# Performance work log

Hardware: AMD Instinct MI355X
Metric: run time of the kernel (lower is better)

Reference implementation:

```python
import jax, jax.numpy as jnp
import numpy as np

HEADS = 8
NEG_SLOPE = 0.2  # PyG GATConv default LeakyReLU slope


def _gat_layer(x, src, dst, W, a_src, a_dst, bias, heads, out_ch):
    """PyG-style GATConv (concat heads, self-loops already appended, eval mode).
    x: [N, F_in]; src/dst: [E_tot] int; W: [F_in, heads*out_ch];
    a_src/a_dst: [heads, out_ch]; bias: [heads*out_ch].
    """
    N = x.shape[0]
    h = (x @ W).reshape(N, heads, out_ch)                      # [N, H, C]
    # per-node attention logits (gathered per edge as scalars, not features)
    al_s = jnp.einsum('nhc,hc->nh', h, a_src)                  # [N, H]
    al_d = jnp.einsum('nhc,hc->nh', h, a_dst)                  # [N, H]
    e = jax.nn.leaky_relu(al_s[src] + al_d[dst], negative_slope=NEG_SLOPE)  # [E, H]
    # segment softmax over incoming edges of each target node (stable)
    e_max = jax.ops.segment_max(e, dst, num_segments=N)        # self-loops => no empty segments
    ex = jnp.exp(e - e_max[dst])
    denom = jax.ops.segment_sum(ex, dst, num_segments=N)
    alpha = ex / (denom[dst] + 1e-16)                          # [E, H]
    # gather source features, weight, scatter-add to targets
    out = jax.ops.segment_sum(h[src] * alpha[:, :, None], dst, num_segments=N)  # [N, H, C]
    return out.reshape(N, heads * out_ch) + bias


def setup_inputs() -> dict:
    key = jax.random.key(0)
    ks = jax.random.split(key, 16)
    N, E, F_IN, NUM_CLASSES = 50000, 1600000, 128, 16
    s = 0.1
    return {
        'x': jax.random.normal(ks[0], (N, F_IN), dtype=jnp.float32),
        'edge_index': jax.random.randint(ks[1], (2, E), 0, N, dtype=jnp.int64),
        # GAT layer 1: 128 -> 8 heads x 8
        'W1': jax.random.normal(ks[2], (F_IN, 64), dtype=jnp.float32) * s,
        'a1_src': jax.random.normal(ks[3], (8, 8), dtype=jnp.float32) * s,
        'a1_dst': jax.random.normal(ks[4], (8, 8), dtype=jnp.float32) * s,
        'b1': jnp.zeros((64,), dtype=jnp.float32),
        # GAT layer 2: 64 -> 8 heads x 4
        'W2': jax.random.normal(ks[5], (64, 32), dtype=jnp.float32) * s,
        'a2_src': jax.random.normal(ks[6], (8, 4), dtype=jnp.float32) * s,
        'a2_dst': jax.random.normal(ks[7], (8, 4), dtype=jnp.float32) * s,
        'b2': jnp.zeros((32,), dtype=jnp.float32),
        # torch MultiheadAttention(32, 8): packed in_proj [96,32], out_proj [32,32]
        'in_proj_w': jax.random.normal(ks[8], (96, 32), dtype=jnp.float32) * s,
        'in_proj_b': jnp.zeros((96,), dtype=jnp.float32),
        'out_proj_w': jax.random.normal(ks[9], (32, 32), dtype=jnp.float32) * s,
        'out_proj_b': jnp.zeros((32,), dtype=jnp.float32),
        # fc: 32 -> num_classes
        'fc_w': jax.random.normal(ks[10], (NUM_CLASSES, 32), dtype=jnp.float32) * s,
        'fc_b': jnp.zeros((NUM_CLASSES,), dtype=jnp.float32),
    }


def reference(x, edge_index, W1, a1_src, a1_dst, b1, W2, a2_src, a2_dst, b2,
              in_proj_w, in_proj_b, out_proj_w, out_proj_b, fc_w, fc_b):
    N = x.shape[0]
    loops = jnp.arange(N, dtype=edge_index.dtype)
    src = jnp.concatenate([edge_index[0], loops])  # PyG add_self_loops=True
    dst = jnp.concatenate([edge_index[1], loops])

    h = jax.nn.elu(_gat_layer(x, src, dst, W1, a1_src, a1_dst, b1, HEADS, 8))   # [N, 64]
    h = jax.nn.elu(_gat_layer(h, src, dst, W2, a2_src, a2_dst, b2, HEADS, 4))   # [N, 32]

    # MultiheadAttention on h.unsqueeze(0): shape [1, N, 32] with torch's
    # seq-first layout => seq_len = 1, batch = N. Softmax over a single key
    # is identically 1 for every head, so out = out_proj(v_proj(h)).
    v = h @ in_proj_w[64:96].T + in_proj_b[64:96]   # v-projection slice of packed in_proj
    h = v @ out_proj_w.T + out_proj_b               # [N, 32]

    logits = h @ fc_w.T + fc_b                      # [N, num_classes]
    return jax.nn.log_softmax(logits, axis=1)
```

## Files before the change

### kernel.cpp

```cpp
#include <hip/hip_runtime.h>
#include <hip/hip_bf16.h>
#include <math.h>


#define BSHIFT 7
#define BMASK  ((1 << BSHIFT) - 1)
#define MAXNB  512
#define TILE   8192
#define XST    136
#define SMBYTES 36864

typedef __attribute__((ext_vector_type(8))) short short8;
typedef __attribute__((ext_vector_type(4))) float floatx4;
typedef __attribute__((ext_vector_type(2))) float floatx2;

__device__ __forceinline__ unsigned short f2bf(float f) {
    union { float f; unsigned int u; } v; v.f = f;
    unsigned int u = v.u;
    return (unsigned short)((u + 0x7FFFu + ((u >> 16) & 1u)) >> 16);
}
__device__ __forceinline__ float lrelu(float e) { return fmaxf(e, 0.2f * e); }
__device__ __forceinline__ float elu(float o) {
    return (o > 0.f) ? o : (__expf(o) - 1.f);
}

__global__ __launch_bounds__(256) void fused_pre_kernel(
    const float* __restrict__ x, const float* __restrict__ W,
    const float* __restrict__ a_src, const float* __restrict__ a_dst,
    char* __restrict__ rec1, float* __restrict__ ald, int N, int GB,
    const int* __restrict__ ei, int E, int Et, int NB, int CAP,
    int* __restrict__ gcount, unsigned int* __restrict__ rec, int NT,
    const float* __restrict__ in_proj_w, const float* __restrict__ in_proj_b,
    const float* __restrict__ out_proj_w, const float* __restrict__ out_proj_b,
    const float* __restrict__ fc_w, const float* __restrict__ fc_b,
    float* __restrict__ M, float* __restrict__ bf) {
    __shared__ __align__(16) char sm[SMBYTES];
    int t = threadIdx.x;
    int bid = blockIdx.x;
    if (bid < GB) {
        unsigned short* xs = (unsigned short*)sm;
        unsigned short* wt = xs + 64 * XST;
        int nb = bid * 64;
#pragma unroll
        for (int r = 0; r < 8; ++r) {
            int p = t + 256 * r;
            int row = p >> 5;
            int c4  = p & 31;
            int n = nb + row;
            float4 v = (n < N) ? ((const float4*)x)[(size_t)n * 32 + c4]
                               : make_float4(0.f, 0.f, 0.f, 0.f);
            unsigned short* dst = &xs[row * XST + c4 * 4];
            dst[0] = f2bf(v.x); dst[1] = f2bf(v.y);
            dst[2] = f2bf(v.z); dst[3] = f2bf(v.w);
        }
        {
            int n = t & 63, kg = t >> 6;
#pragma unroll
            for (int c = 0; c < 4; ++c) {
                int k0 = kg * 32 + c * 8;
                unsigned short* dst = &wt[n * XST + k0];
#pragma unroll
                for (int j = 0; j < 8; ++j)
                    dst[j] = f2bf(W[(k0 + j) * 64 + n]);
            }
        }
        __syncthreads();
        int wave = t >> 6, lane = t & 63;
        int m16 = lane & 15, quad = lane >> 4;
        floatx4 acc[4];
#pragma unroll
        for (int i = 0; i < 4; ++i) acc[i] = (floatx4){0.f, 0.f, 0.f, 0.f};
#pragma unroll
        for (int k = 0; k < 4; ++k) {
            int koff = k * 32 + quad * 8;
            short8 afrag = *(const short8*)&xs[(wave * 16 + m16) * XST + koff];
#pragma unroll
            for (int nt = 0; nt < 4; ++nt) {
                short8 bfrag = *(const short8*)&wt[(nt * 16 + m16) * XST + koff];
                acc[nt] = __builtin_amdgcn_mfma_f32_16x16x32_bf16(afrag, bfrag, acc[nt], 0, 0, 0);
            }
        }
        __syncthreads();
        float* hs = (float*)sm;
#pragma unroll
        for (int nt = 0; nt < 4; ++nt)
#pragma unroll
            for (int r = 0; r < 4; ++r)
                hs[(wave * 16 + quad * 4 + r) * 65 + nt * 16 + m16] = acc[nt][r];
        __syncthreads();
        float asv = a_src[lane], adv = a_dst[lane];
        for (int itn = 0; itn < 16; ++itn) {
            int nl = wave * 16 + itn;
            int n = nb + nl;
            if (n >= N) break;
            float v = hs[nl * 65 + lane];
            float ps = v * asv, pd = v * adv;
            ps += __shfl_xor(ps, 1); ps += __shfl_xor(ps, 2); ps += __shfl_xor(ps, 4);
            pd += __shfl_xor(pd, 1); pd += __shfl_xor(pd, 2); pd += __shfl_xor(pd, 4);
            if ((lane & 7) == 0) {
                *(float*)(rec1 + (size_t)n * 128 + 4 * (lane >> 3)) = ps;
                ald[n * 8 + (lane >> 3)] = pd;
            }
            if (lane < 16) {
                const float* hr = &hs[nl * 65 + lane * 4];
                int pk = __builtin_amdgcn_cvt_pk_fp8_f32(hr[0], hr[1], 0, false);
                pk = __builtin_amdgcn_cvt_pk_fp8_f32(hr[2], hr[3], pk, true);
                *(unsigned*)(rec1 + (size_t)n * 128 + 64 + 4 * lane) = (unsigned)pk;
            }
        }
    } else if (bid < GB + NT) {
        unsigned int* lrec = (unsigned int*)sm;
        int* h   = (int*)(sm + TILE * 4);
        int* cur = (int*)(sm + TILE * 4 + MAXNB * 4);
        for (int i = t; i < NB; i += 256) h[i] = 0;
        int tile0 = (bid - GB) * TILE;
        int cnt = Et - tile0; if (cnt > TILE) cnt = TILE;
        __syncthreads();
        for (int j = t; j < cnt; j += 256) {
            int jj = tile0 + j;
            int srcv, d;
            if (jj < E) { srcv = ei[jj]; d = ei[E + jj]; } else { srcv = jj - E; d = jj - E; }
            lrec[j] = (unsigned)srcv | ((unsigned)d << 16);
            atomicAdd(&h[d >> BSHIFT], 1);
        }
        __syncthreads();
        for (int i = t; i < NB; i += 256)
            cur[i] = h[i] ? atomicAdd(&gcount[i], h[i]) : 0;
        __syncthreads();
        for (int j = t; j < cnt; j += 256) {
            unsigned v = lrec[j];
            int b = v >> (16 + BSHIFT);
            int pos = atomicAdd(&cur[b], 1);
            if (pos < CAP)
                rec[(size_t)b * CAP + pos] =
                    (v & 0xFFFFu) | ((((v >> 16) & BMASK)) << 16);
        }
    } else {
        float* Wvo = (float*)sm;
        float* bvo = (float*)(sm + 4096);
        const float* Wv = in_proj_w + 64 * 32;
        const float* bv = in_proj_b + 64;
        for (int idx = t; idx < 1024; idx += 256) {
            int i = idx >> 5, j = idx & 31;
            float acc = 0.f;
            for (int k = 0; k < 32; ++k) acc += out_proj_w[i * 32 + k] * Wv[k * 32 + j];
            Wvo[idx] = acc;
        }
        if (t < 32) {
            float acc = 0.f;
            for (int k = 0; k < 32; ++k) acc += out_proj_w[t * 32 + k] * bv[k];
            bvo[t] = acc + out_proj_b[t];
        }
        __syncthreads();
        for (int idx = t; idx < 16 * 32; idx += 256) {
            int cc = idx >> 5, j = idx & 31;
            float acc = 0.f;
            for (int i = 0; i < 32; ++i) acc += fc_w[cc * 32 + i] * Wvo[i * 32 + j];
            M[idx] = acc;
        }
        if (t < 16) {
            float acc = 0.f;
            for (int i = 0; i < 32; ++i) acc += fc_w[t * 32 + i] * bvo[i];
            bf[t] = acc + fc_b[t];
        }
    }
}

__global__ __launch_bounds__(256) void csr_finalize_kernel(
    const unsigned int* __restrict__ rec, const int* __restrict__ gcount,
    int* __restrict__ rowp, unsigned short* __restrict__ esrc,
    int N, int Et, int CAP) {
    __shared__ int h[128];
    __shared__ int nb[128];
    __shared__ int cur[128];
    __shared__ int ssum[256];
    int b = blockIdx.x, t = threadIdx.x;
    size_t rbase = (size_t)b * CAP;
    int cnt = gcount[b]; if (cnt > CAP) cnt = CAP;
    if (t < 128) h[t] = 0;
    int acc = 0;
    for (int i = t; i < b; i += 256) {
        int v = gcount[i];
        acc += (v < CAP) ? v : CAP;
    }
    ssum[t] = acc;
    __syncthreads();
    for (int off = 128; off >= 1; off >>= 1) {
        if (t < off) ssum[t] += ssum[t + off];
        __syncthreads();
    }
    int obase = ssum[0];
    for (int i = t; i < cnt; i += 256)
        atomicAdd(&h[(rec[rbase + i] >> 16) & 127], 1);
    __syncthreads();
    if (t == 0) {
        int run = obase;
        for (int i = 0; i < 128; ++i) { nb[i] = run; run += h[i]; }
    }
    __syncthreads();
    if (t < 128) cur[t] = nb[t];
    int n0 = b << BSHIFT;
    if (t < 128 && n0 + t < N) rowp[n0 + t] = nb[t];
    if (b == 0 && t == 0) rowp[N] = Et;
    __syncthreads();
    for (int i = t; i < cnt; i += 256) {
        unsigned r = rec[rbase + i];
        int pos = atomicAdd(&cur[(r >> 16) & 127], 1);
        esrc[pos] = (unsigned short)(r & 0xFFFFu);
    }
}

__global__ __launch_bounds__(256) void gat_agg64_g2_kernel(
    const int* __restrict__ rowp, const unsigned short* __restrict__ esrc,
    const char* __restrict__ rec1, const float* __restrict__ ald_arr,
    const float* __restrict__ bias,
    const float* __restrict__ W2, const float* __restrict__ a2s,
    const float* __restrict__ a2d,
    char* __restrict__ rec2, float* __restrict__ ald2, int N) {
    __shared__ __align__(16) float W2p[2][8][32][4];
    __shared__ __align__(16) float oL[4][64];
    __shared__ __align__(16) float h2L[4][32];
    int t = threadIdx.x;
    for (int idx = t; idx < 2048; idx += 256) {
        int k = idx >> 5, l = idx & 31;
        W2p[k >> 5][(k & 31) >> 2][l][k & 3] = W2[idx];
    }
    __syncthreads();
    const int lane = t & 63;
    const int wv = t >> 6;
    const int e = lane >> 4;
    const int c = lane & 15;
    const int hd = c >> 1;
    const int aoff = 4 * hd;
    const int foff = 64 + 4 * c;
    int n = blockIdx.x * 4 + wv;
    if (n >= N) return;
    float aldv = ald_arr[n * 8 + hd];
    int beg = rowp[n], end = rowp[n + 1];
    float dA = 0.f, dB = 0.f;
    floatx2 p0a = {0.f, 0.f}, p0b = {0.f, 0.f};
    floatx2 p1a = {0.f, 0.f}, p1b = {0.f, 0.f};
    floatx2 p2a = {0.f, 0.f}, p2b = {0.f, 0.f};
    floatx2 p3a = {0.f, 0.f}, p3b = {0.f, 0.f};
    int i = beg;
    for (; i + 32 <= end; i += 32) {
        int s0 = esrc[i + e],      s1 = esrc[i + 4 + e];
        int s2 = esrc[i + 8 + e],  s3 = esrc[i + 12 + e];
        int s4 = esrc[i + 16 + e], s5 = esrc[i + 20 + e];
        int s6 = esrc[i + 24 + e], s7 = esrc[i + 28 + e];
        const char* r0 = rec1 + (size_t)s0 * 128;
        const char* r1 = rec1 + (size_t)s1 * 128;
        const char* r2 = rec1 + (size_t)s2 * 128;
        const char* r3 = rec1 + (size_t)s3 * 128;
        const char* r4 = rec1 + (size_t)s4 * 128;
        const char* r5 = rec1 + (size_t)s5 * 128;
        const char* r6 = rec1 + (size_t)s6 * 128;
        const char* r7 = rec1 + (size_t)s7 * 128;
        float e0 = *(const float*)(r0 + aoff), e1 = *(const float*)(r1 + aoff);
        float e2 = *(const float*)(r2 + aoff), e3 = *(const float*)(r3 + aoff);
        float e4 = *(const float*)(r4 + aoff), e5 = *(const float*)(r5 + aoff);
        float e6 = *(const float*)(r6 + aoff), e7 = *(const float*)(r7 + aoff);
        unsigned g0 = *(const unsigned*)(r0 + foff), g1 = *(const unsigned*)(r1 + foff);
        unsigned g2 = *(const unsigned*)(r2 + foff), g3 = *(const unsigned*)(r3 + foff);
        unsigned g4 = *(const unsigned*)(r4 + foff), g5 = *(const unsigned*)(r5 + foff);
        unsigned g6 = *(const unsigned*)(r6 + foff), g7 = *(const unsigned*)(r7 + foff);
        float w0 = __expf(lrelu(e0 + aldv));
        float w1 = __expf(lrelu(e1 + aldv));
        float w2 = __expf(lrelu(e2 + aldv));
        float w3 = __expf(lrelu(e3 + aldv));
        float w4 = __expf(lrelu(e4 + aldv));
        float w5 = __expf(lrelu(e5 + aldv));
        float w6 = __expf(lrelu(e6 + aldv));
        float w7 = __expf(lrelu(e7 + aldv));
        dA += w0 + w2; dB += w1 + w3;
        dA += w4 + w6; dB += w5 + w7;
        p0a += w0 * __builtin_amdgcn_cvt_pk_f32_fp8(g0, false);
        p0b += w0 * __builtin_amdgcn_cvt_pk_f32_fp8(g0, true);
        p1a += w1 * __builtin_amdgcn_cvt_pk_f32_fp8(g1, false);
        p1b += w1 * __builtin_amdgcn_cvt_pk_f32_fp8(g1, true);
        p2a += w2 * __builtin_amdgcn_cvt_pk_f32_fp8(g2, false);
        p2b += w2 * __builtin_amdgcn_cvt_pk_f32_fp8(g2, true);
        p3a += w3 * __builtin_amdgcn_cvt_pk_f32_fp8(g3, false);
        p3b += w3 * __builtin_amdgcn_cvt_pk_f32_fp8(g3, true);
        p0a += w4 * __builtin_amdgcn_cvt_pk_f32_fp8(g4, false);
        p0b += w4 * __builtin_amdgcn_cvt_pk_f32_fp8(g4, true);
        p1a += w5 * __builtin_amdgcn_cvt_pk_f32_fp8(g5, false);
        p1b += w5 * __builtin_amdgcn_cvt_pk_f32_fp8(g5, true);
        p2a += w6 * __builtin_amdgcn_cvt_pk_f32_fp8(g6, false);
        p2b += w6 * __builtin_amdgcn_cvt_pk_f32_fp8(g6, true);
        p3a += w7 * __builtin_amdgcn_cvt_pk_f32_fp8(g7, false);
        p3b += w7 * __builtin_amdgcn_cvt_pk_f32_fp8(g7, true);
    }
    for (; i < end; i += 16) {
        int i0 = i + e, i1 = i + 4 + e, i2 = i + 8 + e, i3 = i + 12 + e;
        bool v0 = i0 < end, v1 = i1 < end, v2 = i2 < end, v3 = i3 < end;
        int c0 = v0 ? i0 : beg;
        int c1 = v1 ? i1 : beg;
        int c2 = v2 ? i2 : beg;
        int c3 = v3 ? i3 : beg;
        int s0 = esrc[c0], s1 = esrc[c1], s2 = esrc[c2], s3 = esrc[c3];
        const char* r0 = rec1 + (size_t)s0 * 128;
        const char* r1 = rec1 + (size_t)s1 * 128;
        const char* r2 = rec1 + (size_t)s2 * 128;
        const char* r3 = rec1 + (size_t)s3 * 128;
        float e0 = *(const float*)(r0 + aoff), e1 = *(const float*)(r1 + aoff);
        float e2 = *(const float*)(r2 + aoff), e3 = *(const float*)(r3 + aoff);
        unsigned g0 = *(const unsigned*)(r0 + foff), g1 = *(const unsigned*)(r1 + foff);
        unsigned g2 = *(const unsigned*)(r2 + foff), g3 = *(const unsigned*)(r3 + foff);
        float w0 = v0 ? __expf(lrelu(e0 + aldv)) : 0.f;
        float w1 = v1 ? __expf(lrelu(e1 + aldv)) : 0.f;
        float w2 = v2 ? __expf(lrelu(e2 + aldv)) : 0.f;
        float w3 = v3 ? __expf(lrelu(e3 + aldv)) : 0.f;
        dA += w0 + w2; dB += w1 + w3;
        p0a += w0 * __builtin_amdgcn_cvt_pk_f32_fp8(g0, false);
        p0b += w0 * __builtin_amdgcn_cvt_pk_f32_fp8(g0, true);
        p1a += w1 * __builtin_amdgcn_cvt_pk_f32_fp8(g1, false);
        p1b += w1 * __builtin_amdgcn_cvt_pk_f32_fp8(g1, true);
        p2a += w2 * __builtin_amdgcn_cvt_pk_f32_fp8(g2, false);
        p2b += w2 * __builtin_amdgcn_cvt_pk_f32_fp8(g2, true);
        p3a += w3 * __builtin_amdgcn_cvt_pk_f32_fp8(g3, false);
        p3b += w3 * __builtin_amdgcn_cvt_pk_f32_fp8(g3, true);
    }
    float d = dA + dB;
    floatx2 Pa = (p0a + p1a) + (p2a + p3a);
    floatx2 Pb = (p0b + p1b) + (p2b + p3b);
    float P0 = Pa.x, P1 = Pa.y, P2 = Pb.x, P3 = Pb.y;
    d  += __shfl_xor(d, 16);  d  += __shfl_xor(d, 32);
    P0 += __shfl_xor(P0, 16); P0 += __shfl_xor(P0, 32);
    P1 += __shfl_xor(P1, 16); P1 += __shfl_xor(P1, 32);
    P2 += __shfl_xor(P2, 16); P2 += __shfl_xor(P2, 32);
    P3 += __shfl_xor(P3, 16); P3 += __shfl_xor(P3, 32);
    float inv = 1.f / (d + 1e-16f);
    float4 bv = ((const float4*)bias)[c];
    float o0 = elu(P0 * inv + bv.x);
    float o1 = elu(P1 * inv + bv.y);
    float o2 = elu(P2 * inv + bv.z);
    float o3 = elu(P3 * inv + bv.w);
    if (lane < 16) *(float4*)&oL[wv][c * 4] = make_float4(o0, o1, o2, o3);
    const int l = lane & 31, kh = lane >> 5;
    const float* orow = &oL[wv][kh * 32];
    float a0 = 0.f, a1 = 0.f, a2 = 0.f, a3 = 0.f;
#pragma unroll
    for (int g = 0; g < 8; ++g) {
        float4 ov = *(const float4*)&orow[g * 4];
        float4 wv4 = *(const float4*)&W2p[kh][g][l][0];
        a0 += ov.x * wv4.x; a1 += ov.y * wv4.y;
        a2 += ov.z * wv4.z; a3 += ov.w * wv4.w;
    }
    float acc = (a0 + a1) + (a2 + a3);
    acc += __shfl_xor(acc, 32);
    float ps = acc * a2s[l], pd = acc * a2d[l];
    ps += __shfl_xor(ps, 1); ps += __shfl_xor(ps, 2);
    pd += __shfl_xor(pd, 1); pd += __shfl_xor(pd, 2);
    if (lane < 32) {
        h2L[wv][l] = acc;
        if ((l & 3) == 0) {
            *(float*)(rec2 + (size_t)n * 64 + 4 * (l >> 2)) = ps;
            ald2[n * 8 + (l >> 2)] = pd;
        }
    }
    if (lane < 8) {
        const float* hr = &h2L[wv][lane * 4];
        int pk = __builtin_amdgcn_cvt_pk_fp8_f32(hr[0], hr[1], 0, false);
        pk = __builtin_amdgcn_cvt_pk_fp8_f32(hr[2], hr[3], pk, true);
        *(unsigned*)(rec2 + (size_t)n * 64 + 32 + 4 * lane) = (unsigned)pk;
    }
}

__global__ __launch_bounds__(256) void gat_agg32_fin_kernel(
    const int* __restrict__ rowp, const unsigned short* __restrict__ esrc,
    const char* __restrict__ rec2, const float* __restrict__ ald_arr,
    const float* __restrict__ bias,
    const float* __restrict__ M, const float* __restrict__ bf,
    float* __restrict__ out, int N) {
    __shared__ __align__(16) float Mp[8][16][4];
    __shared__ float bfs[16];
    __shared__ __align__(16) float oL[4][32];
    int t = threadIdx.x;
    for (int i = t; i < 512; i += 256) {
        int j = i >> 5, k = i & 31;
        Mp[k >> 2][j][k & 3] = M[i];
    }
    if (t < 16) bfs[t] = bf[t];
    __syncthreads();
    const int lane = t & 63;
    const int wv = t >> 6;
    const int e = lane >> 3;
    const int c = lane & 7;
    const int aoff = 4 * c;
    const int foff = 32 + 4 * c;
    int n = blockIdx.x * 4 + wv;
    if (n >= N) return;
    float aldv = ald_arr[n * 8 + c];
    int beg = rowp[n], end = rowp[n + 1];
    float d0 = 0.f, d1 = 0.f, d2 = 0.f, d3 = 0.f;
    floatx2 p0a = {0.f, 0.f}, p0b = {0.f, 0.f};
    floatx2 p1a = {0.f, 0.f}, p1b = {0.f, 0.f};
    floatx2 p2a = {0.f, 0.f}, p2b = {0.f, 0.f};
    floatx2 p3a = {0.f, 0.f}, p3b = {0.f, 0.f};
    int base = beg;
    for (; base + 32 <= end; base += 32) {
        int s0 = esrc[base + e],      s1 = esrc[base + 8 + e];
        int s2 = esrc[base + 16 + e], s3 = esrc[base + 24 + e];
        const char* r0 = rec2 + (size_t)s0 * 64;
        const char* r1 = rec2 + (size_t)s1 * 64;
        const char* r2 = rec2 + (size_t)s2 * 64;
        const char* r3 = rec2 + (size_t)s3 * 64;
        float e0 = *(const float*)(r0 + aoff) + aldv;
        float e1 = *(const float*)(r1 + aoff) + aldv;
        float e2 = *(const float*)(r2 + aoff) + aldv;
        float e3 = *(const float*)(r3 + aoff) + aldv;
        unsigned g0 = *(const unsigned*)(r0 + foff);
        unsigned g1 = *(const unsigned*)(r1 + foff);
        unsigned g2 = *(const unsigned*)(r2 + foff);
        unsigned g3 = *(const unsigned*)(r3 + foff);
        float w0 = __expf(lrelu(e0));
        float w1 = __expf(lrelu(e1));
        float w2 = __expf(lrelu(e2));
        float w3 = __expf(lrelu(e3));
        d0 += w0; d1 += w1; d2 += w2; d3 += w3;
        p0a += w0 * __builtin_amdgcn_cvt_pk_f32_fp8(g0, false);
        p0b += w0 * __builtin_amdgcn_cvt_pk_f32_fp8(g0, true);
        p1a += w1 * __builtin_amdgcn_cvt_pk_f32_fp8(g1, false);
        p1b += w1 * __builtin_amdgcn_cvt_pk_f32_fp8(g1, true);
        p2a += w2 * __builtin_amdgcn_cvt_pk_f32_fp8(g2, false);
        p2b += w2 * __builtin_amdgcn_cvt_pk_f32_fp8(g2, true);
        p3a += w3 * __builtin_amdgcn_cvt_pk_f32_fp8(g3, false);
        p3b += w3 * __builtin_amdgcn_cvt_pk_f32_fp8(g3, true);
    }
    for (; base < end; base += 32) {
        int i0 = base + e;
        int i1 = base + 8 + e;
        int i2 = base + 16 + e;
        int i3 = base + 24 + e;
        bool v0 = i0 < end, v1 = i1 < end, v2 = i2 < end, v3 = i3 < end;
        int c0 = v0 ? i0 : beg;
        int c1 = v1 ? i1 : beg;
        int c2 = v2 ? i2 : beg;
        int c3 = v3 ? i3 : beg;
        int s0 = esrc[c0], s1 = esrc[c1], s2 = esrc[c2], s3 = esrc[c3];
        const char* r0 = rec2 + (size_t)s0 * 64;
        const char* r1 = rec2 + (size_t)s1 * 64;
        const char* r2 = rec2 + (size_t)s2 * 64;
        const char* r3 = rec2 + (size_t)s3 * 64;
        float e0 = *(const float*)(r0 + aoff) + aldv;
        float e1 = *(const float*)(r1 + aoff) + aldv;
        float e2 = *(const float*)(r2 + aoff) + aldv;
        float e3 = *(const float*)(r3 + aoff) + aldv;
        unsigned g0 = *(const unsigned*)(r0 + foff);
        unsigned g1 = *(const unsigned*)(r1 + foff);
        unsigned g2 = *(const unsigned*)(r2 + foff);
        unsigned g3 = *(const unsigned*)(r3 + foff);
        float w0 = v0 ? __expf(lrelu(e0)) : 0.f;
        float w1 = v1 ? __expf(lrelu(e1)) : 0.f;
        float w2 = v2 ? __expf(lrelu(e2)) : 0.f;
        float w3 = v3 ? __expf(lrelu(e3)) : 0.f;
        d0 += w0; d1 += w1; d2 += w2; d3 += w3;
        p0a += w0 * __builtin_amdgcn_cvt_pk_f32_fp8(g0, false);
        p0b += w0 * __builtin_amdgcn_cvt_pk_f32_fp8(g0, true);
        p1a += w1 * __builtin_amdgcn_cvt_pk_f32_fp8(g1, false);
        p1b += w1 * __builtin_amdgcn_cvt_pk_f32_fp8(g1, true);
        p2a += w2 * __builtin_amdgcn_cvt_pk_f32_fp8(g2, false);
        p2b += w2 * __builtin_amdgcn_cvt_pk_f32_fp8(g2, true);
        p3a += w3 * __builtin_amdgcn_cvt_pk_f32_fp8(g3, false);
        p3b += w3 * __builtin_amdgcn_cvt_pk_f32_fp8(g3, true);
    }
    float d = (d0 + d1) + (d2 + d3);
    floatx2 Pa = (p0a + p1a) + (p2a + p3a);
    floatx2 Pb = (p0b + p1b) + (p2b + p3b);
    float P0 = Pa.x, P1 = Pa.y, P2 = Pb.x, P3 = Pb.y;
    d  += __shfl_xor(d, 8);  d  += __shfl_xor(d, 16);  d  += __shfl_xor(d, 32);
    P0 += __shfl_xor(P0, 8); P0 += __shfl_xor(P0, 16); P0 += __shfl_xor(P0, 32);
    P1 += __shfl_xor(P1, 8); P1 += __shfl_xor(P1, 16); P1 += __shfl_xor(P1, 32);
    P2 += __shfl_xor(P2, 8); P2 += __shfl_xor(P2, 16); P2 += __shfl_xor(P2, 32);
    P3 += __shfl_xor(P3, 8); P3 += __shfl_xor(P3, 16); P3 += __shfl_xor(P3, 32);
    float inv = 1.f / (d + 1e-16f);
    float4 bv = ((const float4*)bias)[c];
    float o0 = elu(P0 * inv + bv.x);
    float o1 = elu(P1 * inv + bv.y);
    float o2 = elu(P2 * inv + bv.z);
    float o3 = elu(P3 * inv + bv.w);
    if (lane < 8) *(float4*)&oL[wv][c * 4] = make_float4(o0, o1, o2, o3);
    const int j = lane & 15;
    const float* orow = oL[wv];
    float a0 = 0.f, a1 = 0.f, a2 = 0.f, a3 = 0.f;
#pragma unroll
    for (int g = 0; g < 8; ++g) {
        float4 ov = *(const float4*)&orow[g * 4];
        float4 mv = *(const float4*)&Mp[g][j][0];
        a0 += ov.x * mv.x; a1 += ov.y * mv.y;
        a2 += ov.z * mv.z; a3 += ov.w * mv.w;
    }
    float logit = (a0 + a1) + (a2 + a3) + bfs[j];
    float mx = logit;
    mx = fmaxf(mx, __shfl_xor(mx, 1));
    mx = fmaxf(mx, __shfl_xor(mx, 2));
    mx = fmaxf(mx, __shfl_xor(mx, 4));
    mx = fmaxf(mx, __shfl_xor(mx, 8));
    float ex = __expf(logit - mx);
    float se = ex;
    se += __shfl_xor(se, 1);
    se += __shfl_xor(se, 2);
    se += __shfl_xor(se, 4);
    se += __shfl_xor(se, 8);
    float res = logit - (mx + __logf(se));
    if (lane < 16) out[(size_t)n * 16 + j] = res;
}

extern "C" void kernel_launch(void* const* d_in, const int* in_sizes, int n_in,
                              void* d_out, int out_size, void* d_ws, size_t ws_size,
                              hipStream_t stream) {
    const float* x   = (const float*)d_in[0];
    const int*   ei  = (const int*)d_in[1];
    const float* W1  = (const float*)d_in[2];
    const float* a1s = (const float*)d_in[3];
    const float* a1d = (const float*)d_in[4];
    const float* b1  = (const float*)d_in[5];
    const float* W2  = (const float*)d_in[6];
    const float* a2s = (const float*)d_in[7];
    const float* a2d = (const float*)d_in[8];
    const float* b2  = (const float*)d_in[9];
    const float* ipw = (const float*)d_in[10];
    const float* ipb = (const float*)d_in[11];
    const float* opw = (const float*)d_in[12];
    const float* opb = (const float*)d_in[13];
    const float* fcw = (const float*)d_in[14];
    const float* fcb = (const float*)d_in[15];
    float* out = (float*)d_out;

    int N = in_sizes[0] / 128;
    int E = in_sizes[1] / 2;
    int Et = E + N;
    int NB = (N + BMASK) >> BSHIFT;
    int NTILES = (Et + TILE - 1) / TILE;
    int GB = (N + 63) / 64;
    int CAP = Et / NB;
    CAP = CAP + CAP / 8 + 256;
    CAP = (CAP + 255) & ~255;

    char* ws = (char*)d_ws;
    size_t off = 0;
    auto alloc = [&](size_t bytes) -> void* {
        void* p = ws + off;
        off += bytes;
        off = (off + 255) & ~(size_t)255;
        return p;
    };
    int*   bcount = (int*)alloc(MAXNB * 4);
    unsigned int*   rec  = (unsigned int*)alloc((size_t)NB * CAP * 4);
    int*   rowp   = (int*)alloc((size_t)(N + 1) * 4);
    unsigned short* esrc = (unsigned short*)alloc((size_t)Et * 2);
    char* rec1   = (char*)alloc((size_t)N * 128);
    float* al1d  = (float*)alloc((size_t)N * 8 * 4);
    char* rec2   = (char*)alloc((size_t)N * 64);
    float* al2d  = (float*)alloc((size_t)N * 8 * 4);
    float* Mf    = (float*)alloc(512 * 4);
    float* bff   = (float*)alloc(16 * 4);
    (void)ws_size; (void)n_in; (void)out_size;

    hipMemsetAsync(bcount, 0, MAXNB * 4, stream);
    fused_pre_kernel<<<GB + NTILES + 1, 256, 0, stream>>>(
        x, W1, a1s, a1d, rec1, al1d, N, GB,
        ei, E, Et, NB, CAP, bcount, rec, NTILES,
        ipw, ipb, opw, opb, fcw, fcb, Mf, bff);
    csr_finalize_kernel<<<NB, 256, 0, stream>>>(rec, bcount, rowp, esrc, N, Et, CAP);

    gat_agg64_g2_kernel<<<(N + 3) / 4, 256, 0, stream>>>(
        rowp, esrc, rec1, al1d, b1, W2, a2s, a2d, rec2, al2d, N);
    gat_agg32_fin_kernel<<<(N + 3) / 4, 256, 0, stream>>>(
        rowp, esrc, rec2, al2d, b2, Mf, bff, out, N);
}
```

Before: 211.9 us.

## Split layer-1 node records, stage CSR scatter in LDS, add low-degree fast paths

Layer-1 per-node data moves from one interleaved 128-byte record into separate arrays for the source logits and the packed fp8 features. The CSR finalize step now sorts edge sources into a shared-memory buffer and writes them out contiguously instead of scattering straight to global memory. Both aggregation kernels gain a fully unrolled path for nodes of degree up to 48 or 64 that issues all gathers at once for more memory-level parallelism. The LDS buffer caps the per-bucket CAP, so an overfull bucket could lose edges, and the unrolled paths raise register use.

```diff
diff --git a/kernel.cpp b/kernel.cpp
--- a/kernel.cpp
+++ b/kernel.cpp
@@ -9,6 +9,7 @@
 #define TILE   8192
 #define XST    136
 #define SMBYTES 36864
+#define LESRC_MAX 6144
 
 typedef __attribute__((ext_vector_type(8))) short short8;
 typedef __attribute__((ext_vector_type(4))) float floatx4;
@@ -27,7 +28,8 @@
 __global__ __launch_bounds__(256) void fused_pre_kernel(
     const float* __restrict__ x, const float* __restrict__ W,
     const float* __restrict__ a_src, const float* __restrict__ a_dst,
-    char* __restrict__ rec1, float* __restrict__ ald, int N, int GB,
+    unsigned int* __restrict__ h1p, float* __restrict__ als,
+    float* __restrict__ ald, int N, int GB,
     const int* __restrict__ ei, int E, int Et, int NB, int CAP,
     int* __restrict__ gcount, unsigned int* __restrict__ rec, int NT,
     const float* __restrict__ in_proj_w, const float* __restrict__ in_proj_b,
@@ -98,14 +100,14 @@
             ps += __shfl_xor(ps, 1); ps += __shfl_xor(ps, 2); ps += __shfl_xor(ps, 4);
             pd += __shfl_xor(pd, 1); pd += __shfl_xor(pd, 2); pd += __shfl_xor(pd, 4);
             if ((lane & 7) == 0) {
-                *(float*)(rec1 + (size_t)n * 128 + 4 * (lane >> 3)) = ps;
+                als[n * 8 + (lane >> 3)] = ps;
                 ald[n * 8 + (lane >> 3)] = pd;
             }
             if (lane < 16) {
                 const float* hr = &hs[nl * 65 + lane * 4];
                 int pk = __builtin_amdgcn_cvt_pk_fp8_f32(hr[0], hr[1], 0, false);
                 pk = __builtin_amdgcn_cvt_pk_fp8_f32(hr[2], hr[3], pk, true);
-                *(unsigned*)(rec1 + (size_t)n * 128 + 64 + 4 * lane) = (unsigned)pk;
+                h1p[(size_t)n * 16 + lane] = (unsigned)pk;
             }
         }
     } else if (bid < GB + NT) {
@@ -174,6 +176,7 @@
     __shared__ int nb[128];
     __shared__ int cur[128];
     __shared__ int ssum[256];
+    __shared__ unsigned short lesrc[LESRC_MAX];
     int b = blockIdx.x, t = threadIdx.x;
     size_t rbase = (size_t)b * CAP;
     int cnt = gcount[b]; if (cnt > CAP) cnt = CAP;
@@ -194,26 +197,29 @@
         atomicAdd(&h[(rec[rbase + i] >> 16) & 127], 1);
     __syncthreads();
     if (t == 0) {
-        int run = obase;
+        int run = 0;
         for (int i = 0; i < 128; ++i) { nb[i] = run; run += h[i]; }
     }
     __syncthreads();
     if (t < 128) cur[t] = nb[t];
     int n0 = b << BSHIFT;
-    if (t < 128 && n0 + t < N) rowp[n0 + t] = nb[t];
+    if (t < 128 && n0 + t < N) rowp[n0 + t] = obase + nb[t];
     if (b == 0 && t == 0) rowp[N] = Et;
     __syncthreads();
     for (int i = t; i < cnt; i += 256) {
         unsigned r = rec[rbase + i];
         int pos = atomicAdd(&cur[(r >> 16) & 127], 1);
-        esrc[pos] = (unsigned short)(r & 0xFFFFu);
-    }
+        lesrc[pos] = (unsigned short)(r & 0xFFFFu);
+    }
+    __syncthreads();
+    for (int i = t; i < cnt; i += 256)
+        esrc[obase + i] = lesrc[i];
 }
 
 __global__ __launch_bounds__(256) void gat_agg64_g2_kernel(
     const int* __restrict__ rowp, const unsigned short* __restrict__ esrc,
-    const char* __restrict__ rec1, const float* __restrict__ ald_arr,
-    const float* __restrict__ bias,
+    const unsigned int* __restrict__ feat, const float* __restrict__ als,
+    const float* __restrict__ ald_arr, const float* __restrict__ bias,
     const float* __restrict__ W2, const float* __restrict__ a2s,
     const float* __restrict__ a2d,
     char* __restrict__ rec2, float* __restrict__ ald2, int N) {
@@ -231,95 +237,120 @@
     const int e = lane >> 4;
     const int c = lane & 15;
     const int hd = c >> 1;
-    const int aoff = 4 * hd;
-    const int foff = 64 + 4 * c;
     int n = blockIdx.x * 4 + wv;
     if (n >= N) return;
     float aldv = ald_arr[n * 8 + hd];
     int beg = rowp[n], end = rowp[n + 1];
+    int deg = end - beg;
     float dA = 0.f, dB = 0.f;
     floatx2 p0a = {0.f, 0.f}, p0b = {0.f, 0.f};
     floatx2 p1a = {0.f, 0.f}, p1b = {0.f, 0.f};
     floatx2 p2a = {0.f, 0.f}, p2b = {0.f, 0.f};
     floatx2 p3a = {0.f, 0.f}, p3b = {0.f, 0.f};
-    int i = beg;
-    for (; i + 32 <= end; i += 32) {
-        int s0 = esrc[i + e],      s1 = esrc[i + 4 + e];
-        int s2 = esrc[i + 8 + e],  s3 = esrc[i + 12 + e];
-        int s4 = esrc[i + 16 + e], s5 = esrc[i + 20 + e];
-        int s6 = esrc[i + 24 + e], s7 = esrc[i + 28 + e];
-        const char* r0 = rec1 + (size_t)s0 * 128;
-        const char* r1 = rec1 + (size_t)s1 * 128;
-        const char* r2 = rec1 + (size_t)s2 * 128;
-        const char* r3 = rec1 + (size_t)s3 * 128;
-        const char* r4 = rec1 + (size_t)s4 * 128;
-        const char* r5 = rec1 + (size_t)s5 * 128;
-        const char* r6 = rec1 + (size_t)s6 * 128;
-        const char* r7 = rec1 + (size_t)s7 * 128;
-        float e0 = *(const float*)(r0 + aoff), e1 = *(const float*)(r1 + aoff);
-        float e2 = *(const float*)(r2 + aoff), e3 = *(const float*)(r3 + aoff);
-        float e4 = *(const float*)(r4 + aoff), e5 = *(const float*)(r5 + aoff);
-        float e6 = *(const float*)(r6 + aoff), e7 = *(const float*)(r7 + aoff);
-        unsigned g0 = *(const unsigned*)(r0 + foff), g1 = *(const unsigned*)(r1 + foff);
-        unsigned g2 = *(const unsigned*)(r2 + foff), g3 = *(const unsigned*)(r3 + foff);
-        unsigned g4 = *(const unsigned*)(r4 + foff), g5 = *(const unsigned*)(r5 + foff);
-        unsigned g6 = *(const unsigned*)(r6 + foff), g7 = *(const unsigned*)(r7 + foff);
-        float w0 = __expf(lrelu(e0 + aldv));
-        float w1 = __expf(lrelu(e1 + aldv));
-        float w2 = __expf(lrelu(e2 + aldv));
-        float w3 = __expf(lrelu(e3 + aldv));
-        float w4 = __expf(lrelu(e4 + aldv));
-        float w5 = __expf(lrelu(e5 + aldv));
-        float w6 = __expf(lrelu(e6 + aldv));
-        float w7 = __expf(lrelu(e7 + aldv));
-        dA += w0 + w2; dB += w1 + w3;
-        dA += w4 + w6; dB += w5 + w7;
-        p0a += w0 * __builtin_amdgcn_cvt_pk_f32_fp8(g0, false);
-        p0b += w0 * __builtin_amdgcn_cvt_pk_f32_fp8(g0, true);
-        p1a += w1 * __builtin_amdgcn_cvt_pk_f32_fp8(g1, false);
-        p1b += w1 * __builtin_amdgcn_cvt_pk_f32_fp8(g1, true);
-        p2a += w2 * __builtin_amdgcn_cvt_pk_f32_fp8(g2, false);
-        p2b += w2 * __builtin_amdgcn_cvt_pk_f32_fp8(g2, true);
-        p3a += w3 * __builtin_amdgcn_cvt_pk_f32_fp8(g3, false);
-        p3b += w3 * __builtin_amdgcn_cvt_pk_f32_fp8(g3, true);
-        p0a += w4 * __builtin_amdgcn_cvt_pk_f32_fp8(g4, false);
-        p0b += w4 * __builtin_amdgcn_cvt_pk_f32_fp8(g4, true);
-        p1a += w5 * __builtin_amdgcn_cvt_pk_f32_fp8(g5, false);
-        p1b += w5 * __builtin_amdgcn_cvt_pk_f32_fp8(g5, true);
-        p2a += w6 * __builtin_amdgcn_cvt_pk_f32_fp8(g6, false);
-        p2b += w6 * __builtin_amdgcn_cvt_pk_f32_fp8(g6, true);
-        p3a += w7 * __builtin_amdgcn_cvt_pk_f32_fp8(g7, false);
-        p3b += w7 * __builtin_amdgcn_cvt_pk_f32_fp8(g7, true);
-    }
-    for (; i < end; i += 16) {
-        int i0 = i + e, i1 = i + 4 + e, i2 = i + 8 + e, i3 = i + 12 + e;
-        bool v0 = i0 < end, v1 = i1 < end, v2 = i2 < end, v3 = i3 < end;
-        int c0 = v0 ? i0 : beg;
-        int c1 = v1 ? i1 : beg;
-        int c2 = v2 ? i2 : beg;
-        int c3 = v3 ? i3 : beg;
-        int s0 = esrc[c0], s1 = esrc[c1], s2 = esrc[c2], s3 = esrc[c3];
-        const char* r0 = rec1 + (size_t)s0 * 128;
-        const char* r1 = rec1 + (size_t)s1 * 128;
-        const char* r2 = rec1 + (size_t)s2 * 128;
-        const char* r3 = rec1 + (size_t)s3 * 128;
-        float e0 = *(const float*)(r0 + aoff), e1 = *(const float*)(r1 + aoff);
-        float e2 = *(const float*)(r2 + aoff), e3 = *(const float*)(r3 + aoff);
-        unsigned g0 = *(const unsigned*)(r0 + foff), g1 = *(const unsigned*)(r1 + foff);
-        unsigned g2 = *(const unsigned*)(r2 + foff), g3 = *(const unsigned*)(r3 + foff);
-        float w0 = v0 ? __expf(lrelu(e0 + aldv)) : 0.f;
-        float w1 = v1 ? __expf(lrelu(e1 + aldv)) : 0.f;
-        float w2 = v2 ? __expf(lrelu(e2 + aldv)) : 0.f;
-        float w3 = v3 ? __expf(lrelu(e3 + aldv)) : 0.f;
-        dA += w0 + w2; dB += w1 + w3;
-        p0a += w0 * __builtin_amdgcn_cvt_pk_f32_fp8(g0, false);
-        p0b += w0 * __builtin_amdgcn_cvt_pk_f32_fp8(g0, true);
-        p1a += w1 * __builtin_amdgcn_cvt_pk_f32_fp8(g1, false);
-        p1b += w1 * __builtin_amdgcn_cvt_pk_f32_fp8(g1, true);
-        p2a += w2 * __builtin_amdgcn_cvt_pk_f32_fp8(g2, false);
-        p2b += w2 * __builtin_amdgcn_cvt_pk_f32_fp8(g2, true);
-        p3a += w3 * __builtin_amdgcn_cvt_pk_f32_fp8(g3, false);
-        p3b += w3 * __builtin_amdgcn_cvt_pk_f32_fp8(g3, true);
+    if (deg <= 48) {
+        int s[12];
+#pragma unroll
+        for (int g = 0; g < 12; ++g) {
+            int p = beg + g * 4 + e;
+            s[g] = esrc[(p < end) ? p : beg];
+        }
+        float ev[12];
+        unsigned gg[12];
+#pragma unroll
+        for (int g = 0; g < 12; ++g) {
+            ev[g] = als[s[g] * 8 + hd];
+            gg[g] = feat[s[g] * 16 + c];
+        }
+#pragma unroll
+        for (int g = 0; g < 12; ++g) {
+            bool vv = (beg + g * 4 + e) < end;
+            float w = vv ? __expf(lrelu(ev[g] + aldv)) : 0.f;
+            if ((g & 3) == 0) {
+                dA += w;
+                p0a += w * __builtin_amdgcn_cvt_pk_f32_fp8(gg[g], false);
+                p0b += w * __builtin_amdgcn_cvt_pk_f32_fp8(gg[g], true);
+            } else if ((g & 3) == 1) {
+                dB += w;
+                p1a += w * __builtin_amdgcn_cvt_pk_f32_fp8(gg[g], false);
+                p1b += w * __builtin_amdgcn_cvt_pk_f32_fp8(gg[g], true);
+            } else if ((g & 3) == 2) {
+                dA += w;
+                p2a += w * __builtin_amdgcn_cvt_pk_f32_fp8(gg[g], false);
+                p2b += w * __builtin_amdgcn_cvt_pk_f32_fp8(gg[g], true);
+            } else {
+                dB += w;
+                p3a += w * __builtin_amdgcn_cvt_pk_f32_fp8(gg[g], false);
+                p3b += w * __builtin_amdgcn_cvt_pk_f32_fp8(gg[g], true);
+            }
+        }
+    } else {
+        int i = beg;
+        for (; i + 32 <= end; i += 32) {
+            int s0 = esrc[i + e],      s1 = esrc[i + 4 + e];
+            int s2 = esrc[i + 8 + e],  s3 = esrc[i + 12 + e];
+            int s4 = esrc[i + 16 + e], s5 = esrc[i + 20 + e];
+            int s6 = esrc[i + 24 + e], s7 = esrc[i + 28 + e];
+            float e0 = als[s0 * 8 + hd], e1 = als[s1 * 8 + hd];
+            float e2 = als[s2 * 8 + hd], e3 = als[s3 * 8 + hd];
+            float e4 = als[s4 * 8 + hd], e5 = als[s5 * 8 + hd];
+            float e6 = als[s6 * 8 + hd], e7 = als[s7 * 8 + hd];
+            unsigned g0 = feat[s0 * 16 + c], g1 = feat[s1 * 16 + c];
+            unsigned g2 = feat[s2 * 16 + c], g3 = feat[s3 * 16 + c];
+            unsigned g4 = feat[s4 * 16 + c], g5 = feat[s5 * 16 + c];
+            unsigned g6 = feat[s6 * 16 + c], g7 = feat[s7 * 16 + c];
+            float w0 = __expf(lrelu(e0 + aldv));
+            float w1 = __expf(lrelu(e1 + aldv));
+            float w2 = __expf(lrelu(e2 + aldv));
+            float w3 = __expf(lrelu(e3 + aldv));
+            float w4 = __expf(lrelu(e4 + aldv));
+            float w5 = __expf(lrelu(e5 + aldv));
+            float w6 = __expf(lrelu(e6 + aldv));
+            float w7 = __expf(lrelu(e7 + aldv));
+            dA += w0 + w2; dB += w1 + w3;
+            dA += w4 + w6; dB += w5 + w7;
+            p0a += w0 * __builtin_amdgcn_cvt_pk_f32_fp8(g0, false);
+            p0b += w0 * __builtin_amdgcn_cvt_pk_f32_fp8(g0, true);
+            p1a += w1 * __builtin_amdgcn_cvt_pk_f32_fp8(g1, false);
+            p1b += w1 * __builtin_amdgcn_cvt_pk_f32_fp8(g1, true);
+            p2a += w2 * __builtin_amdgcn_cvt_pk_f32_fp8(g2, false);
+            p2b += w2 * __builtin_amdgcn_cvt_pk_f32_fp8(g2, true);
+            p3a += w3 * __builtin_amdgcn_cvt_pk_f32_fp8(g3, false);
+            p3b += w3 * __builtin_amdgcn_cvt_pk_f32_fp8(g3, true);
+            p0a += w4 * __builtin_amdgcn_cvt_pk_f32_fp8(g4, false);
+            p0b += w4 * __builtin_amdgcn_cvt_pk_f32_fp8(g4, true);
+            p1a += w5 * __builtin_amdgcn_cvt_pk_f32_fp8(g5, false);
+            p1b += w5 * __builtin_amdgcn_cvt_pk_f32_fp8(g5, true);
+            p2a += w6 * __builtin_amdgcn_cvt_pk_f32_fp8(g6, false);
+            p2b += w6 * __builtin_amdgcn_cvt_pk_f32_fp8(g6, true);
+            p3a += w7 * __builtin_amdgcn_cvt_pk_f32_fp8(g7, false);
+            p3b += w7 * __builtin_amdgcn_cvt_pk_f32_fp8(g7, true);
+        }
+        for (; i < end; i += 16) {
+            int i0 = i + e, i1 = i + 4 + e, i2 = i + 8 + e, i3 = i + 12 + e;
+            bool v0 = i0 < end, v1 = i1 < end, v2 = i2 < end, v3 = i3 < end;
+            int c0 = v0 ? i0 : beg;
+            int c1 = v1 ? i1 : beg;
+            int c2 = v2 ? i2 : beg;
+            int c3 = v3 ? i3 : beg;
+            int s0 = esrc[c0], s1 = esrc[c1], s2 = esrc[c2], s3 = esrc[c3];
+            float e0 = als[s0 * 8 + hd], e1 = als[s1 * 8 + hd];
+            float e2 = als[s2 * 8 + hd], e3 = als[s3 * 8 + hd];
+            unsigned g0 = feat[s0 * 16 + c], g1 = feat[s1 * 16 + c];
+            unsigned g2 = feat[s2 * 16 + c], g3 = feat[s3 * 16 + c];
+            float w0 = v0 ? __expf(lrelu(e0 + aldv)) : 0.f;
+            float w1 = v1 ? __expf(lrelu(e1 + aldv)) : 0.f;
+            float w2 = v2 ? __expf(lrelu(e2 + aldv)) : 0.f;
+            float w3 = v3 ? __expf(lrelu(e3 + aldv)) : 0.f;
+            dA += w0 + w2; dB += w1 + w3;
+            p0a += w0 * __builtin_amdgcn_cvt_pk_f32_fp8(g0, false);
+            p0b += w0 * __builtin_amdgcn_cvt_pk_f32_fp8(g0, true);
+            p1a += w1 * __builtin_amdgcn_cvt_pk_f32_fp8(g1, false);
+            p1b += w1 * __builtin_amdgcn_cvt_pk_f32_fp8(g1, true);
+            p2a += w2 * __builtin_amdgcn_cvt_pk_f32_fp8(g2, false);
+            p2b += w2 * __builtin_amdgcn_cvt_pk_f32_fp8(g2, true);
+            p3a += w3 * __builtin_amdgcn_cvt_pk_f32_fp8(g3, false);
+            p3b += w3 * __builtin_amdgcn_cvt_pk_f32_fp8(g3, true);
+        }
     }
     float d = dA + dB;
     floatx2 Pa = (p0a + p1a) + (p2a + p3a);
@@ -393,77 +424,117 @@
     if (n >= N) return;
     float aldv = ald_arr[n * 8 + c];
     int beg = rowp[n], end = rowp[n + 1];
+    int deg = end - beg;
     float d0 = 0.f, d1 = 0.f, d2 = 0.f, d3 = 0.f;
     floatx2 p0a = {0.f, 0.f}, p0b = {0.f, 0.f};
     floatx2 p1a = {0.f, 0.f}, p1b = {0.f, 0.f};
     floatx2 p2a = {0.f, 0.f}, p2b = {0.f, 0.f};
     floatx2 p3a = {0.f, 0.f}, p3b = {0.f, 0.f};
-    int base = beg;
-    for (; base + 32 <= end; base += 32) {
-        int s0 = esrc[base + e],      s1 = esrc[base + 8 + e];
-        int s2 = esrc[base + 16 + e], s3 = esrc[base + 24 + e];
-        const char* r0 = rec2 + (size_t)s0 * 64;
-        const char* r1 = rec2 + (size_t)s1 * 64;
-        const char* r2 = rec2 + (size_t)s2 * 64;
-        const char* r3 = rec2 + (size_t)s3 * 64;
-        float e0 = *(const float*)(r0 + aoff) + aldv;
-        float e1 = *(const float*)(r1 + aoff) + aldv;
-        float e2 = *(const float*)(r2 + aoff) + aldv;
-        float e3 = *(const float*)(r3 + aoff) + aldv;
-        unsigned g0 = *(const unsigned*)(r0 + foff);
-        unsigned g1 = *(const unsigned*)(r1 + foff);
-        unsigned g2 = *(const unsigned*)(r2 + foff);
-        unsigned g3 = *(const unsigned*)(r3 + foff);
-        float w0 = __expf(lrelu(e0));
-        float w1 = __expf(lrelu(e1));
-        float w2 = __expf(lrelu(e2));
-        float w3 = __expf(lrelu(e3));
-        d0 += w0; d1 += w1; d2 += w2; d3 += w3;
-        p0a += w0 * __builtin_amdgcn_cvt_pk_f32_fp8(g0, false);
-        p0b += w0 * __builtin_amdgcn_cvt_pk_f32_fp8(g0, true);
-        p1a += w1 * __builtin_amdgcn_cvt_pk_f32_fp8(g1, false);
-        p1b += w1 * __builtin_amdgcn_cvt_pk_f32_fp8(g1, true);
-        p2a += w2 * __builtin_amdgcn_cvt_pk_f32_fp8(g2, false);
-        p2b += w2 * __builtin_amdgcn_cvt_pk_f32_fp8(g2, true);
-        p3a += w3 * __builtin_amdgcn_cvt_pk_f32_fp8(g3, false);
-        p3b += w3 * __builtin_amdgcn_cvt_pk_f32_fp8(g3, true);
-    }
-    for (; base < end; base += 32) {
-        int i0 = base + e;
-        int i1 = base + 8 + e;
-        int i2 = base + 16 + e;
-        int i3 = base + 24 + e;
-        bool v0 = i0 < end, v1 = i1 < end, v2 = i2 < end, v3 = i3 < end;
-        int c0 = v0 ? i0 : beg;
-        int c1 = v1 ? i1 : beg;
-        int c2 = v2 ? i2 : beg;
-        int c3 = v3 ? i3 : beg;
-        int s0 = esrc[c0], s1 = esrc[c1], s2 = esrc[c2], s3 = esrc[c3];
-        const char* r0 = rec2 + (size_t)s0 * 64;
-        const char* r1 = rec2 + (size_t)s1 * 64;
-        const char* r2 = rec2 + (size_t)s2 * 64;
-        const char* r3 = rec2 + (size_t)s3 * 64;
-        float e0 = *(const float*)(r0 + aoff) + aldv;
-        float e1 = *(const float*)(r1 + aoff) + aldv;
-        float e2 = *(const float*)(r2 + aoff) + aldv;
-        float e3 = *(const float*)(r3 + aoff) + aldv;
-        unsigned g0 = *(const unsigned*)(r0 + foff);
-        unsigned g1 = *(const unsigned*)(r1 + foff);
-        unsigned g2 = *(const unsigned*)(r2 + foff);
-        unsigned g3 = *(const unsigned*)(r3 + foff);
-        float w0 = v0 ? __expf(lrelu(e0)) : 0.f;
-        float w1 = v1 ? __expf(lrelu(e1)) : 0.f;
-        float w2 = v2 ? __expf(lrelu(e2)) : 0.f;
-        float w3 = v3 ? __expf(lrelu(e3)) : 0.f;
-        d0 += w0; d1 += w1; d2 += w2; d3 += w3;
-        p0a += w0 * __builtin_amdgcn_cvt_pk_f32_fp8(g0, false);
-        p0b += w0 * __builtin_amdgcn_cvt_pk_f32_fp8(g0, true);
-        p1a += w1 * __builtin_amdgcn_cvt_pk_f32_fp8(g1, false);
-        p1b += w1 * __builtin_amdgcn_cvt_pk_f32_fp8(g1, true);
-        p2a += w2 * __builtin_amdgcn_cvt_pk_f32_fp8(g2, false);
-        p2b += w2 * __builtin_amdgcn_cvt_pk_f32_fp8(g2, true);
-        p3a += w3 * __builtin_amdgcn_cvt_pk_f32_fp8(g3, false);
-        p3b += w3 * __builtin_amdgcn_cvt_pk_f32_fp8(g3, true);
+    if (deg <= 64) {
+        int s[8];
+#pragma unroll
+        for (int g = 0; g < 8; ++g) {
+            int p = beg + g * 8 + e;
+            s[g] = esrc[(p < end) ? p : beg];
+        }
+        float ev[8];
+        unsigned gg[8];
+#pragma unroll
+        for (int g = 0; g < 8; ++g) {
+            const char* r = rec2 + (size_t)s[g] * 64;
+            ev[g] = *(const float*)(r + aoff);
+            gg[g] = *(const unsigned*)(r + foff);
+        }
+#pragma unroll
+        for (int g = 0; g < 8; ++g) {
+            bool vv = (beg + g * 8 + e) < end;
+            float w = vv ? __expf(lrelu(ev[g] + aldv)) : 0.f;
+            if ((g & 3) == 0) {
+                d0 += w;
+                p0a += w * __builtin_amdgcn_cvt_pk_f32_fp8(gg[g], false);
+                p0b += w * __builtin_amdgcn_cvt_pk_f32_fp8(gg[g], true);
+            } else if ((g & 3) == 1) {
+                d1 += w;
+                p1a += w * __builtin_amdgcn_cvt_pk_f32_fp8(gg[g], false);
+                p1b += w * __builtin_amdgcn_cvt_pk_f32_fp8(gg[g], true);
+            } else if ((g & 3) == 2) {
+                d2 += w;
+                p2a += w * __builtin_amdgcn_cvt_pk_f32_fp8(gg[g], false);
+                p2b += w * __builtin_amdgcn_cvt_pk_f32_fp8(gg[g], true);
+            } else {
+                d3 += w;
+                p3a += w * __builtin_amdgcn_cvt_pk_f32_fp8(gg[g], false);
+                p3b += w * __builtin_amdgcn_cvt_pk_f32_fp8(gg[g], true);
+            }
+        }
+    } else {
+        int base = beg;
+        for (; base + 32 <= end; base += 32) {
+            int s0 = esrc[base + e],      s1 = esrc[base + 8 + e];
+            int s2 = esrc[base + 16 + e], s3 = esrc[base + 24 + e];
+            const char* r0 = rec2 + (size_t)s0 * 64;
+            const char* r1 = rec2 + (size_t)s1 * 64;
+            const char* r2 = rec2 + (size_t)s2 * 64;
+            const char* r3 = rec2 + (size_t)s3 * 64;
+            float e0 = *(const float*)(r0 + aoff) + aldv;
+            float e1 = *(const float*)(r1 + aoff) + aldv;
+            float e2 = *(const float*)(r2 + aoff) + aldv;
+            float e3 = *(const float*)(r3 + aoff) + aldv;
+            unsigned g0 = *(const unsigned*)(r0 + foff);
+            unsigned g1 = *(const unsigned*)(r1 + foff);
+            unsigned g2 = *(const unsigned*)(r2 + foff);
+            unsigned g3 = *(const unsigned*)(r3 + foff);
+            float w0 = __expf(lrelu(e0));
+            float w1 = __expf(lrelu(e1));
+            float w2 = __expf(lrelu(e2));
+            float w3 = __expf(lrelu(e3));
+            d0 += w0; d1 += w1; d2 += w2; d3 += w3;
+            p0a += w0 * __builtin_amdgcn_cvt_pk_f32_fp8(g0, false);
+            p0b += w0 * __builtin_amdgcn_cvt_pk_f32_fp8(g0, true);
+            p1a += w1 * __builtin_amdgcn_cvt_pk_f32_fp8(g1, false);
+            p1b += w1 * __builtin_amdgcn_cvt_pk_f32_fp8(g1, true);
+            p2a += w2 * __builtin_amdgcn_cvt_pk_f32_fp8(g2, false);
+            p2b += w2 * __builtin_amdgcn_cvt_pk_f32_fp8(g2, true);
+            p3a += w3 * __builtin_amdgcn_cvt_pk_f32_fp8(g3, false);
+            p3b += w3 * __builtin_amdgcn_cvt_pk_f32_fp8(g3, true);
+        }
+        for (; base < end; base += 32) {
+            int i0 = base + e;
+            int i1 = base + 8 + e;
+            int i2 = base + 16 + e;
+            int i3 = base + 24 + e;
+            bool v0 = i0 < end, v1 = i1 < end, v2 = i2 < end, v3 = i3 < end;
+            int c0 = v0 ? i0 : beg;
+            int c1 = v1 ? i1 : beg;
+            int c2 = v2 ? i2 : beg;
+            int c3 = v3 ? i3 : beg;
+            int s0 = esrc[c0], s1 = esrc[c1], s2 = esrc[c2], s3 = esrc[c3];
+            const char* r0 = rec2 + (size_t)s0 * 64;
+            const char* r1 = rec2 + (size_t)s1 * 64;
+            const char* r2 = rec2 + (size_t)s2 * 64;
+            const char* r3 = rec2 + (size_t)s3 * 64;
+            float e0 = *(const float*)(r0 + aoff) + aldv;
+            float e1 = *(const float*)(r1 + aoff) + aldv;
+            float e2 = *(const float*)(r2 + aoff) + aldv;
+            float e3 = *(const float*)(r3 + aoff) + aldv;
+            unsigned g0 = *(const unsigned*)(r0 + foff);
+            unsigned g1 = *(const unsigned*)(r1 + foff);
+            unsigned g2 = *(const unsigned*)(r2 + foff);
+            unsigned g3 = *(const unsigned*)(r3 + foff);
+            float w0 = v0 ? __expf(lrelu(e0)) : 0.f;
+            float w1 = v1 ? __expf(lrelu(e1)) : 0.f;
+            float w2 = v2 ? __expf(lrelu(e2)) : 0.f;
+            float w3 = v3 ? __expf(lrelu(e3)) : 0.f;
+            d0 += w0; d1 += w1; d2 += w2; d3 += w3;
+            p0a += w0 * __builtin_amdgcn_cvt_pk_f32_fp8(g0, false);
+            p0b += w0 * __builtin_amdgcn_cvt_pk_f32_fp8(g0, true);
+            p1a += w1 * __builtin_amdgcn_cvt_pk_f32_fp8(g1, false);
+            p1b += w1 * __builtin_amdgcn_cvt_pk_f32_fp8(g1, true);
+            p2a += w2 * __builtin_amdgcn_cvt_pk_f32_fp8(g2, false);
+            p2b += w2 * __builtin_amdgcn_cvt_pk_f32_fp8(g2, true);
+            p3a += w3 * __builtin_amdgcn_cvt_pk_f32_fp8(g3, false);
+            p3b += w3 * __builtin_amdgcn_cvt_pk_f32_fp8(g3, true);
+        }
     }
     float d = (d0 + d1) + (d2 + d3);
     floatx2 Pa = (p0a + p1a) + (p2a + p3a);
@@ -537,6 +608,7 @@
     int CAP = Et / NB;
     CAP = CAP + CAP / 8 + 256;
     CAP = (CAP + 255) & ~255;
+    if (CAP > LESRC_MAX) CAP = LESRC_MAX;
 
     char* ws = (char*)d_ws;
     size_t off = 0;
@@ -550,7 +622,8 @@
     unsigned int*   rec  = (unsigned int*)alloc((size_t)NB * CAP * 4);
     int*   rowp   = (int*)alloc((size_t)(N + 1) * 4);
     unsigned short* esrc = (unsigned short*)alloc((size_t)Et * 2);
-    char* rec1   = (char*)alloc((size_t)N * 128);
+    unsigned int* h1p = (unsigned int*)alloc((size_t)N * 16 * 4);
+    float* al1s  = (float*)alloc((size_t)N * 8 * 4);
     float* al1d  = (float*)alloc((size_t)N * 8 * 4);
     char* rec2   = (char*)alloc((size_t)N * 64);
     float* al2d  = (float*)alloc((size_t)N * 8 * 4);
@@ -560,13 +633,13 @@
 
     hipMemsetAsync(bcount, 0, MAXNB * 4, stream);
     fused_pre_kernel<<<GB + NTILES + 1, 256, 0, stream>>>(
-        x, W1, a1s, a1d, rec1, al1d, N, GB,
+        x, W1, a1s, a1d, h1p, al1s, al1d, N, GB,
         ei, E, Et, NB, CAP, bcount, rec, NTILES,
         ipw, ipb, opw, opb, fcw, fcb, Mf, bff);
     csr_finalize_kernel<<<NB, 256, 0, stream>>>(rec, bcount, rowp, esrc, N, Et, CAP);
 
     gat_agg64_g2_kernel<<<(N + 3) / 4, 256, 0, stream>>>(
-        rowp, esrc, rec1, al1d, b1, W2, a2s, a2d, rec2, al2d, N);
+        rowp, esrc, h1p, al1s, al1d, b1, W2, a2s, a2d, rec2, al2d, N);
     gat_agg32_fin_kernel<<<(N + 3) / 4, 256, 0, stream>>>(
         rowp, esrc, rec2, al2d, b2, Mf, bff, out, N);
 }
```

New measurement: 206.1 us. 1.03x faster.
